# Kernel optimization log

Measured on AMD Instinct MI355X. Metric: run time of the kernel, lower is better.

The kernel has to match this reference:

```python
import jax, jax.numpy as jnp
import numpy as np


def setup_inputs() -> dict:
    key = jax.random.key(0)
    k1, k2 = jax.random.split(key)
    mutation_dist = jax.random.uniform(k1, (8192, 96), dtype=jnp.float32)
    train_data = jax.random.uniform(k2, (65536, 96), dtype=jnp.float32)
    return {"mutation_dist": mutation_dist, "train_data": train_data}


def reference(mutation_dist, train_data):
    # torch.cdist with default p=2: pairwise Euclidean distances [N, M]
    # default compute_mode for large inputs)
    x2 = jnp.sum(mutation_dist * mutation_dist, axis=-1, keepdims=True)   # [N,1]
    y2 = jnp.sum(train_data * train_data, axis=-1)[None, :]               # [1,M]
    xy = mutation_dist @ train_data.T                                     # [N,M]
    sq = jnp.maximum(x2 + y2 - 2.0 * xy, 0.0)
    distances = jnp.sqrt(sq)
    min_dist = jnp.min(distances, axis=1) * 10.0
    return min_dist
```

## Files before the change

kernel.cpp:

```cpp
#include <hip/hip_runtime.h>
#include <hip/hip_bf16.h>


typedef __attribute__((ext_vector_type(8))) short bf16x8;
typedef __attribute__((ext_vector_type(4))) float f32x4;
typedef __attribute__((ext_vector_type(4))) int i32x4;

#define NQ 8192
#define NT 65536
#define KD 96
#define KP 128
#define QB 512
#define TSPLIT 64
#define TCHUNK (NT / TSPLIT)
#define TTILE 64
#define TILES (TCHUNK / TTILE)

#define GLOAD_LDS16(gp, lp)                                                  \
  __builtin_amdgcn_global_load_lds(                                          \
      (const __attribute__((address_space(1))) unsigned int*)(gp),           \
      (__attribute__((address_space(3))) unsigned int*)(lp), 16, 0, 0)
#define GLOAD_LDS4(gp, lp)                                                   \
  __builtin_amdgcn_global_load_lds(                                          \
      (const __attribute__((address_space(1))) unsigned int*)(gp),           \
      (__attribute__((address_space(3))) unsigned int*)(lp), 4, 0, 0)

static __device__ __forceinline__ ushort f2bf(float f) {
  unsigned u = __float_as_uint(f);
  return (ushort)((u + 0x7fffu + ((u >> 16) & 1u)) >> 16);
}
static __device__ __forceinline__ unsigned pk2(float a, float b) {
  return (unsigned)f2bf(a) | ((unsigned)f2bf(b) << 16);
}
static __device__ __forceinline__ int imin(int a, int b) { return a < b ? a : b; }

__global__ __launch_bounds__(256) void prep_kernel(
    const float* __restrict__ qf, const float* __restrict__ tf,
    char* __restrict__ qi8, char* __restrict__ ti8,
    int* __restrict__ x2i, int* __restrict__ y2h,
    float* __restrict__ outp)
{
  const int tid = threadIdx.x;
  const int b = blockIdx.x;
  const bool isq = b < (NQ / 64);
  const int rb = isq ? b : b - (NQ / 64);
  const float4* src = (const float4*)((isq ? qf : tf) + (size_t)rb * 64 * KD);
  char* drow = (isq ? qi8 : ti8) + (size_t)rb * 64 * KP;
  const int rloc = tid >> 2;
  const int t = tid & 3;

  unsigned int* op = (unsigned int*)(drow + (size_t)rloc * KP + t * 24);
  int sn = 0;
  #pragma unroll
  for (int i = 0; i < 6; ++i) {
    float4 v = src[tid * 6 + i];
    int q0 = (int)rintf(v.x * 254.0f) - 127;
    int q1 = (int)rintf(v.y * 254.0f) - 127;
    int q2 = (int)rintf(v.z * 254.0f) - 127;
    int q3 = (int)rintf(v.w * 254.0f) - 127;
    sn += q0 * q0 + q1 * q1 + q2 * q2 + q3 * q3;
    int w0 = isq ? q0 : -q0, w1 = isq ? q1 : -q1;
    int w2 = isq ? q2 : -q2, w3 = isq ? q3 : -q3;
    op[i] = (unsigned)(w0 & 255) | ((unsigned)(w1 & 255) << 8) |
            ((unsigned)(w2 & 255) << 16) | ((unsigned)(w3 & 255) << 24);
  }
  *(uint2*)(drow + (size_t)rloc * KP + 96 + t * 8) = make_uint2(0u, 0u);

  sn += __shfl_xor(sn, 1, 64);
  sn += __shfl_xor(sn, 2, 64);
  if (t == 0) {
    int row = rb * 64 + rloc;
    if (isq) { x2i[row] = sn; outp[row] = __uint_as_float(0x7f800000u); }
    else     { y2h[row] = (sn + 1) >> 1; }
  }
}

__global__ __launch_bounds__(512, 3) void min_dist_kernel(
    const char* __restrict__ qi8, const char* __restrict__ ti8,
    const int* __restrict__ x2i, const int* __restrict__ y2h,
    float* __restrict__ outp)
{
  __shared__ __align__(16) char ldsA[2][TTILE * KP];
  __shared__ __align__(16) int ldsY[2][TTILE];

  const int tid  = threadIdx.x;
  const int w    = tid >> 6;
  const int lane = tid & 63;
  const int quad = lane >> 4;
  const int n    = lane & 15;
  const int tsplit = blockIdx.x & (TSPLIT - 1);
  const int qblock = blockIdx.x / TSPLIT;
  const int qbase  = qblock * QB + w * 64;

  i32x4 bq[4][2];
  #pragma unroll
  for (int ct = 0; ct < 4; ++ct) {
    const char* qp = qi8 + (size_t)(qbase + ct * 16 + n) * KP + quad * 16;
    #pragma unroll
    for (int kh = 0; kh < 2; ++kh)
      bq[ct][kh] = *(const volatile i32x4*)(qp + kh * 64);
  }

  int goff, loff;
  {
    int f = tid >> 6, l = tid & 63;
    int tt = f >> 1, kh = f & 1;
    goff = (tt * 16 + (l & 15)) * KP + kh * 64 + (l >> 4) * 16;
    loff = tid * 16;
  }

  int m0 = 0x7fffffff, m1 = 0x7fffffff, m2 = 0x7fffffff, m3 = 0x7fffffff;

  const int trow0 = tsplit * TCHUNK;

  {
    const char* g0 = ti8 + (size_t)trow0 * KP;
    GLOAD_LDS16(g0 + goff, &ldsA[0][loff]);
    if (w == 0)
      GLOAD_LDS4(y2h + trow0 + lane, &ldsY[0][lane]);
  }
  __syncthreads();

  int cur = 0;
  #pragma unroll 1
  for (int tile = 0; tile < TILES; ++tile) {
    if (tile + 1 < TILES) {
      const int tb2 = trow0 + (tile + 1) * TTILE;
      const char* g2 = ti8 + (size_t)tb2 * KP;
      GLOAD_LDS16(g2 + goff, &ldsA[cur ^ 1][loff]);
      if (w == 0)
        GLOAD_LDS4(y2h + tb2 + lane, &ldsY[cur ^ 1][lane]);
    }

    #pragma unroll
    for (int tt = 0; tt < 4; ++tt) {
      const char* ap = &ldsA[cur][tt * 2048 + lane * 16];
      i32x4 a0 = *(const i32x4*)(ap);
      i32x4 a1 = *(const i32x4*)(ap + 1024);
      i32x4 y2v = *(const i32x4*)&ldsY[cur][tt * 16 + quad * 4];

      i32x4 acc;
      acc = __builtin_amdgcn_mfma_i32_16x16x64_i8(a0, bq[0][0], y2v, 0, 0, 0);
      acc = __builtin_amdgcn_mfma_i32_16x16x64_i8(a1, bq[0][1], acc, 0, 0, 0);
      m0 = imin(m0, imin(imin(acc[0], acc[1]), imin(acc[2], acc[3])));

      acc = __builtin_amdgcn_mfma_i32_16x16x64_i8(a0, bq[1][0], y2v, 0, 0, 0);
      acc = __builtin_amdgcn_mfma_i32_16x16x64_i8(a1, bq[1][1], acc, 0, 0, 0);
      m1 = imin(m1, imin(imin(acc[0], acc[1]), imin(acc[2], acc[3])));

      acc = __builtin_amdgcn_mfma_i32_16x16x64_i8(a0, bq[2][0], y2v, 0, 0, 0);
      acc = __builtin_amdgcn_mfma_i32_16x16x64_i8(a1, bq[2][1], acc, 0, 0, 0);
      m2 = imin(m2, imin(imin(acc[0], acc[1]), imin(acc[2], acc[3])));

      acc = __builtin_amdgcn_mfma_i32_16x16x64_i8(a0, bq[3][0], y2v, 0, 0, 0);
      acc = __builtin_amdgcn_mfma_i32_16x16x64_i8(a1, bq[3][1], acc, 0, 0, 0);
      m3 = imin(m3, imin(imin(acc[0], acc[1]), imin(acc[2], acc[3])));
    }

    __syncthreads();
    cur ^= 1;
  }

  int m[4] = {m0, m1, m2, m3};
  #pragma unroll
  for (int ct = 0; ct < 4; ++ct) {
    m[ct] = imin(m[ct], __shfl_xor(m[ct], 16, 64));
    m[ct] = imin(m[ct], __shfl_xor(m[ct], 32, 64));
  }
  if (quad == 0) {
    #pragma unroll
    for (int ct = 0; ct < 4; ++ct) {
      int q = qbase + ct * 16 + n;
      int sq = x2i[q] + (m[ct] << 1);
      if (sq < 0) sq = 0;
      float val = sqrtf((float)sq) * (10.0f / 254.0f);
      atomicMin((unsigned int*)&outp[q], __float_as_uint(val));
    }
  }
}

extern "C" void kernel_launch(void* const* d_in, const int* in_sizes, int n_in,
                              void* d_out, int out_size, void* d_ws, size_t ws_size,
                              hipStream_t stream) {
  const float* qf = (const float*)d_in[0];
  const float* tf = (const float*)d_in[1];
  float* outp = (float*)d_out;

  char* qi8 = (char*)d_ws;
  char* ti8 = qi8 + (size_t)NQ * KP;
  int* x2i = (int*)(ti8 + (size_t)NT * KP);
  int* y2h = x2i + NQ;

  prep_kernel<<<(NQ + NT) / 64, 256, 0, stream>>>(qf, tf, qi8, ti8, x2i, y2h, outp);
  min_dist_kernel<<<(NQ / QB) * TSPLIT, 512, 0, stream>>>(qi8, ti8, x2i, y2h, outp);
}
```

Before: 127.8 us.

## Switch to 32x32x32 int8 MFMA and drop K padding from 128 to 96

Replaces the 16x16x64 int8 MFMA tiling, which needed K padded to 128, with 32x32x32 int8 MFMAs that cover K=96 exactly in three steps. This removes a quarter of the MFMA work and memory traffic spent on zero padding, and shrinks the int8 buffers and LDS tiles. It also drops the occupancy hint from launch bounds and now uses 16-wide accumulators, which raises register pressure. The min reduction and the final shuffle are reshaped to match the 32-column layout.

Result: faster. 119.3 us (-6.6%).

```diff
diff --git a/kernel.cpp b/kernel.cpp
--- a/kernel.cpp
+++ b/kernel.cpp
@@ -5,11 +5,11 @@
 typedef __attribute__((ext_vector_type(8))) short bf16x8;
 typedef __attribute__((ext_vector_type(4))) float f32x4;
 typedef __attribute__((ext_vector_type(4))) int i32x4;
+typedef __attribute__((ext_vector_type(16))) int i32x16;
 
 #define NQ 8192
 #define NT 65536
 #define KD 96
-#define KP 128
 #define QB 512
 #define TSPLIT 64
 #define TCHUNK (NT / TSPLIT)
@@ -45,11 +45,11 @@
   const bool isq = b < (NQ / 64);
   const int rb = isq ? b : b - (NQ / 64);
   const float4* src = (const float4*)((isq ? qf : tf) + (size_t)rb * 64 * KD);
-  char* drow = (isq ? qi8 : ti8) + (size_t)rb * 64 * KP;
+  char* drow = (isq ? qi8 : ti8) + (size_t)rb * 64 * KD;
   const int rloc = tid >> 2;
   const int t = tid & 3;
 
-  unsigned int* op = (unsigned int*)(drow + (size_t)rloc * KP + t * 24);
+  unsigned pk[6];
   int sn = 0;
   #pragma unroll
   for (int i = 0; i < 6; ++i) {
@@ -61,10 +61,13 @@
     sn += q0 * q0 + q1 * q1 + q2 * q2 + q3 * q3;
     int w0 = isq ? q0 : -q0, w1 = isq ? q1 : -q1;
     int w2 = isq ? q2 : -q2, w3 = isq ? q3 : -q3;
-    op[i] = (unsigned)(w0 & 255) | ((unsigned)(w1 & 255) << 8) |
+    pk[i] = (unsigned)(w0 & 255) | ((unsigned)(w1 & 255) << 8) |
             ((unsigned)(w2 & 255) << 16) | ((unsigned)(w3 & 255) << 24);
   }
-  *(uint2*)(drow + (size_t)rloc * KP + 96 + t * 8) = make_uint2(0u, 0u);
+  uint2* op = (uint2*)(drow + (size_t)rloc * KD + t * 24);
+  op[0] = make_uint2(pk[0], pk[1]);
+  op[1] = make_uint2(pk[2], pk[3]);
+  op[2] = make_uint2(pk[4], pk[5]);
 
   sn += __shfl_xor(sn, 1, 64);
   sn += __shfl_xor(sn, 2, 64);
@@ -75,47 +78,48 @@
   }
 }
 
-__global__ __launch_bounds__(512, 3) void min_dist_kernel(
+__global__ __launch_bounds__(512) void min_dist_kernel(
     const char* __restrict__ qi8, const char* __restrict__ ti8,
     const int* __restrict__ x2i, const int* __restrict__ y2h,
     float* __restrict__ outp)
 {
-  __shared__ __align__(16) char ldsA[2][TTILE * KP];
+  __shared__ __align__(16) char ldsA[2][TTILE * KD];
   __shared__ __align__(16) int ldsY[2][TTILE];
 
   const int tid  = threadIdx.x;
   const int w    = tid >> 6;
   const int lane = tid & 63;
-  const int quad = lane >> 4;
-  const int n    = lane & 15;
+  const int col  = lane & 31;
+  const int hi   = lane >> 5;
   const int tsplit = blockIdx.x & (TSPLIT - 1);
   const int qblock = blockIdx.x / TSPLIT;
   const int qbase  = qblock * QB + w * 64;
 
-  i32x4 bq[4][2];
+  i32x4 bq[2][3];
   #pragma unroll
-  for (int ct = 0; ct < 4; ++ct) {
-    const char* qp = qi8 + (size_t)(qbase + ct * 16 + n) * KP + quad * 16;
+  for (int ct = 0; ct < 2; ++ct) {
+    const char* qp = qi8 + (size_t)(qbase + ct * 32 + col) * KD + hi * 16;
     #pragma unroll
-    for (int kh = 0; kh < 2; ++kh)
-      bq[ct][kh] = *(const volatile i32x4*)(qp + kh * 64);
+    for (int kb = 0; kb < 3; ++kb)
+      bq[ct][kb] = *(const volatile i32x4*)(qp + kb * 32);
   }
 
   int goff, loff;
   {
     int f = tid >> 6, l = tid & 63;
-    int tt = f >> 1, kh = f & 1;
-    goff = (tt * 16 + (l & 15)) * KP + kh * 64 + (l >> 4) * 16;
+    int tt = f / 3, kb = f - tt * 3;
+    goff = (tt * 32 + (l & 31)) * KD + kb * 32 + (l >> 5) * 16;
     loff = tid * 16;
   }
 
-  int m0 = 0x7fffffff, m1 = 0x7fffffff, m2 = 0x7fffffff, m3 = 0x7fffffff;
+  int m0 = 0x7fffffff, m1 = 0x7fffffff;
 
   const int trow0 = tsplit * TCHUNK;
 
   {
-    const char* g0 = ti8 + (size_t)trow0 * KP;
-    GLOAD_LDS16(g0 + goff, &ldsA[0][loff]);
+    const char* g0 = ti8 + (size_t)trow0 * KD;
+    if (tid < 384)
+      GLOAD_LDS16(g0 + goff, &ldsA[0][loff]);
     if (w == 0)
       GLOAD_LDS4(y2h + trow0 + lane, &ldsY[0][lane]);
   }
@@ -126,56 +130,70 @@
   for (int tile = 0; tile < TILES; ++tile) {
     if (tile + 1 < TILES) {
       const int tb2 = trow0 + (tile + 1) * TTILE;
-      const char* g2 = ti8 + (size_t)tb2 * KP;
-      GLOAD_LDS16(g2 + goff, &ldsA[cur ^ 1][loff]);
+      const char* g2 = ti8 + (size_t)tb2 * KD;
+      if (tid < 384)
+        GLOAD_LDS16(g2 + goff, &ldsA[cur ^ 1][loff]);
       if (w == 0)
         GLOAD_LDS4(y2h + tb2 + lane, &ldsY[cur ^ 1][lane]);
     }
 
     #pragma unroll
-    for (int tt = 0; tt < 4; ++tt) {
-      const char* ap = &ldsA[cur][tt * 2048 + lane * 16];
+    for (int tt = 0; tt < 2; ++tt) {
+      const char* ap = &ldsA[cur][tt * 3 * 1024 + lane * 16];
       i32x4 a0 = *(const i32x4*)(ap);
       i32x4 a1 = *(const i32x4*)(ap + 1024);
-      i32x4 y2v = *(const i32x4*)&ldsY[cur][tt * 16 + quad * 4];
-
-      i32x4 acc;
-      acc = __builtin_amdgcn_mfma_i32_16x16x64_i8(a0, bq[0][0], y2v, 0, 0, 0);
-      acc = __builtin_amdgcn_mfma_i32_16x16x64_i8(a1, bq[0][1], acc, 0, 0, 0);
-      m0 = imin(m0, imin(imin(acc[0], acc[1]), imin(acc[2], acc[3])));
-
-      acc = __builtin_amdgcn_mfma_i32_16x16x64_i8(a0, bq[1][0], y2v, 0, 0, 0);
-      acc = __builtin_amdgcn_mfma_i32_16x16x64_i8(a1, bq[1][1], acc, 0, 0, 0);
-      m1 = imin(m1, imin(imin(acc[0], acc[1]), imin(acc[2], acc[3])));
-
-      acc = __builtin_amdgcn_mfma_i32_16x16x64_i8(a0, bq[2][0], y2v, 0, 0, 0);
-      acc = __builtin_amdgcn_mfma_i32_16x16x64_i8(a1, bq[2][1], acc, 0, 0, 0);
-      m2 = imin(m2, imin(imin(acc[0], acc[1]), imin(acc[2], acc[3])));
-
-      acc = __builtin_amdgcn_mfma_i32_16x16x64_i8(a0, bq[3][0], y2v, 0, 0, 0);
-      acc = __builtin_amdgcn_mfma_i32_16x16x64_i8(a1, bq[3][1], acc, 0, 0, 0);
-      m3 = imin(m3, imin(imin(acc[0], acc[1]), imin(acc[2], acc[3])));
+      i32x4 a2 = *(const i32x4*)(ap + 2048);
+
+      i32x4 y0 = *(const i32x4*)&ldsY[cur][tt * 32 + hi * 4];
+      i32x4 y1 = *(const i32x4*)&ldsY[cur][tt * 32 + hi * 4 + 8];
+      i32x4 yq2 = *(const i32x4*)&ldsY[cur][tt * 32 + hi * 4 + 16];
+      i32x4 yq3 = *(const i32x4*)&ldsY[cur][tt * 32 + hi * 4 + 24];
+      i32x16 c;
+      c[0] = y0[0];  c[1] = y0[1];  c[2] = y0[2];  c[3] = y0[3];
+      c[4] = y1[0];  c[5] = y1[1];  c[6] = y1[2];  c[7] = y1[3];
+      c[8] = yq2[0]; c[9] = yq2[1]; c[10] = yq2[2]; c[11] = yq2[3];
+      c[12] = yq3[0]; c[13] = yq3[1]; c[14] = yq3[2]; c[15] = yq3[3];
+
+      i32x16 acc0 = __builtin_amdgcn_mfma_i32_32x32x32_i8(a0, bq[0][0], c, 0, 0, 0);
+      i32x16 acc1 = __builtin_amdgcn_mfma_i32_32x32x32_i8(a0, bq[1][0], c, 0, 0, 0);
+      acc0 = __builtin_amdgcn_mfma_i32_32x32x32_i8(a1, bq[0][1], acc0, 0, 0, 0);
+      acc1 = __builtin_amdgcn_mfma_i32_32x32x32_i8(a1, bq[1][1], acc1, 0, 0, 0);
+      acc0 = __builtin_amdgcn_mfma_i32_32x32x32_i8(a2, bq[0][2], acc0, 0, 0, 0);
+      acc1 = __builtin_amdgcn_mfma_i32_32x32x32_i8(a2, bq[1][2], acc1, 0, 0, 0);
+
+      {
+        int t0 = imin(imin(acc0[0], acc0[1]), imin(acc0[2], acc0[3]));
+        int t1 = imin(imin(acc0[4], acc0[5]), imin(acc0[6], acc0[7]));
+        int t2 = imin(imin(acc0[8], acc0[9]), imin(acc0[10], acc0[11]));
+        int t3 = imin(imin(acc0[12], acc0[13]), imin(acc0[14], acc0[15]));
+        m0 = imin(m0, imin(imin(t0, t1), imin(t2, t3)));
+      }
+      {
+        int t0 = imin(imin(acc1[0], acc1[1]), imin(acc1[2], acc1[3]));
+        int t1 = imin(imin(acc1[4], acc1[5]), imin(acc1[6], acc1[7]));
+        int t2 = imin(imin(acc1[8], acc1[9]), imin(acc1[10], acc1[11]));
+        int t3 = imin(imin(acc1[12], acc1[13]), imin(acc1[14], acc1[15]));
+        m1 = imin(m1, imin(imin(t0, t1), imin(t2, t3)));
+      }
     }
 
     __syncthreads();
     cur ^= 1;
   }
 
-  int m[4] = {m0, m1, m2, m3};
-  #pragma unroll
-  for (int ct = 0; ct < 4; ++ct) {
-    m[ct] = imin(m[ct], __shfl_xor(m[ct], 16, 64));
-    m[ct] = imin(m[ct], __shfl_xor(m[ct], 32, 64));
-  }
-  if (quad == 0) {
-    #pragma unroll
-    for (int ct = 0; ct < 4; ++ct) {
-      int q = qbase + ct * 16 + n;
-      int sq = x2i[q] + (m[ct] << 1);
-      if (sq < 0) sq = 0;
-      float val = sqrtf((float)sq) * (10.0f / 254.0f);
-      atomicMin((unsigned int*)&outp[q], __float_as_uint(val));
-    }
+  m0 = imin(m0, __shfl_xor(m0, 32, 64));
+  m1 = imin(m1, __shfl_xor(m1, 32, 64));
+  if (hi == 0) {
+    int q0 = qbase + col;
+    int sq0 = x2i[q0] + (m0 << 1);
+    if (sq0 < 0) sq0 = 0;
+    atomicMin((unsigned int*)&outp[q0],
+              __float_as_uint(sqrtf((float)sq0) * (10.0f / 254.0f)));
+    int q1 = qbase + 32 + col;
+    int sq1 = x2i[q1] + (m1 << 1);
+    if (sq1 < 0) sq1 = 0;
+    atomicMin((unsigned int*)&outp[q1],
+              __float_as_uint(sqrtf((float)sq1) * (10.0f / 254.0f)));
   }
 }
 
@@ -187,8 +205,8 @@
   float* outp = (float*)d_out;
 
   char* qi8 = (char*)d_ws;
-  char* ti8 = qi8 + (size_t)NQ * KP;
-  int* x2i = (int*)(ti8 + (size_t)NT * KP);
+  char* ti8 = qi8 + (size_t)NQ * KD;
+  int* x2i = (int*)(ti8 + (size_t)NT * KD);
   int* y2h = x2i + NQ;
 
   prep_kernel<<<(NQ + NT) / 64, 256, 0, stream>>>(qf, tf, qi8, ti8, x2i, y2h, outp);
```
